# Optimization experiments

Hardware: AMD Instinct MI355X
Metric: run time of the kernel (lower is better)

Reference implementation:

```python
import jax, jax.numpy as jnp
import numpy as np

L_SEG, M_CHEB, MODES1, MODES2 = 4, 8, 16, 16


def _cft(signals, t_coords, f_points, L, M):
    # signals: [N, C, n] real; returns (real, imag) each [N, C, F]
    n = signals.shape[-1]
    seg_len = 1.0 / L
    starts = jnp.linspace(0.0, 1.0, L + 1)[:-1]                      # [L]
    k = jnp.arange(M, dtype=jnp.float32)
    nodes = -jnp.cos((2.0 * k + 1.0) * jnp.pi / (2.0 * M))           # [M]
    T = jnp.cos(k[:, None] * jnp.arccos(nodes)[None, :])             # [M(k), M(m)]
    w_prime = f_points * (2.0 * jnp.pi * (seg_len / 2.0))            # [F]
    angle = nodes[:, None] * w_prime[None, :]                        # [M, F]
    # quad weights (index k is reused as node index m downstream, as in original)
    Wr = (T @ jnp.cos(angle)) * (seg_len / 2.0)                      # [M, F]
    Wi = (T @ (-jnp.sin(angle))) * (seg_len / 2.0)                   # [M, F] (sign = -1, forward)
    # chebyshev sample points for all segments at once
    t_seg = starts[:, None] + (seg_len / 2.0) * (nodes[None, :] + 1.0)   # [L, M]
    right = jnp.clip(jnp.searchsorted(t_coords, t_seg), 0, n - 1)
    left = jnp.clip(right - 1, 0, n - 1)
    tl, tr = t_coords[left], t_coords[right]
    denom = jnp.where(tr - tl < 1e-8, 1.0, tr - tl)
    wr = (t_seg - tl) / denom
    wl = 1.0 - wr
    seg_sig = wl * signals[..., left] + wr * signals[..., right]     # [N, C, L, M]
    Sr = jnp.einsum('nclm,mf->nclf', seg_sig, Wr)
    Si = jnp.einsum('nclm,mf->nclf', seg_sig, Wi)
    phase = -2.0 * jnp.pi * starts[:, None] * f_points[None, :]      # [L, F]
    cr, ci = jnp.cos(phase), jnp.sin(phase)
    real = jnp.sum(Sr * cr - Si * ci, axis=2)
    imag = jnp.sum(Sr * ci + Si * cr, axis=2)
    return real, imag


def _cft2d(x, m1, m2, L, M):
    B, C, H, W = x.shape
    tw = jnp.linspace(0.0, 1.0, W)
    fw = jnp.fft.rfftfreq(W, d=1.0 / W)[:m2].astype(jnp.float32)
    xr = x.transpose(0, 2, 1, 3).reshape(B * H, C, W)
    r, i = _cft(xr, tw, fw, L, M)                                    # [B*H, C, m2]
    r = r.reshape(B, H, C, m2).transpose(0, 2, 1, 3)                 # [B, C, H, m2]
    i = i.reshape(B, H, C, m2).transpose(0, 2, 1, 3)
    th = jnp.linspace(0.0, 1.0, H)
    fh = jnp.fft.fftfreq(H, d=1.0 / H).astype(jnp.float32)
    hidx = np.concatenate([np.arange(0, m1 // 2), np.arange(H - (m1 - m1 // 2), H)])
    fsel = fh[hidx]
    rh = r.transpose(0, 3, 1, 2).reshape(B * m2, C, H)
    ih = i.transpose(0, 3, 1, 2).reshape(B * m2, C, H)
    rr, ri = _cft(rh, th, fsel, L, M)
    ir, ii = _cft(ih, th, fsel, L, M)
    real = (rr - ii).reshape(B, m2, C, m1).transpose(0, 2, 3, 1)     # [B, C, m1, m2]
    imag = (ri + ir).reshape(B, m2, C, m1).transpose(0, 2, 3, 1)
    return real, imag


def setup_inputs() -> dict:
    key = jax.random.key(0)
    ks = jax.random.split(key, 6)
    B, C, O, H, W = 32, 64, 64, 128, 128
    m1, m2 = MODES1, MODES2
    scale = 1.0 / (C * O)
    x = jax.random.normal(ks[0], (B, C, H, W), jnp.float32)
    w1 = scale * jax.random.uniform(ks[1], (C, O, m1, m2, 2), jnp.float32)
    w2 = scale * jax.random.uniform(ks[2], (C, O, m1, m2, 2), jnp.float32)
    d_in = C * (m1 // 4) * (m2 // 4) * 2
    hid = (C + O) * 2
    lin1_w = jax.random.normal(ks[3], (d_in, hid), jnp.float32) * 0.02
    lin1_b = jnp.zeros((hid,), jnp.float32)
    lin2_w = jax.random.normal(ks[4], (hid, O), jnp.float32) * 0.02
    lin2_b = jnp.zeros((O,), jnp.float32)
    return dict(x=x, w1=w1, w2=w2, lin1_w=lin1_w, lin1_b=lin1_b, lin2_w=lin2_w, lin2_b=lin2_b)


def reference(x, w1, w2, lin1_w, lin1_b, lin2_w, lin2_b):
    m1, m2 = MODES1, MODES2
    B, C, H, W = x.shape
    O = w1.shape[1]
    # FNO spectral conv
    xf = jnp.fft.rfft2(x)                                            # [B, C, H, W//2+1]
    w1c = w1[..., 0] + 1j * w1[..., 1]
    w2c = w2[..., 0] + 1j * w2[..., 1]
    out_ft = jnp.zeros((B, O, H, W // 2 + 1), jnp.complex64)
    out_ft = out_ft.at[:, :, :m1, :m2].set(
        jnp.einsum('bixy,ioxy->boxy', xf[:, :, :m1, :m2], w1c))
    out_ft = out_ft.at[:, :, H - m1:, :m2].set(
        jnp.einsum('bixy,ioxy->boxy', xf[:, :, H - m1:, :m2], w2c))
    x_fno = jnp.fft.irfft2(out_ft, s=(H, W))
    # Chebyshev-quadrature CFT correction path
    cr, ci = _cft2d(x, m1 // 4, m2 // 4, L_SEG, M_CHEB)              # [B, C, m1//4, m2//4]
    flat = jnp.stack([cr, ci], axis=-1).reshape(B, -1)               # view_as_real + flatten(1)
    h = jax.nn.gelu(flat @ lin1_w + lin1_b, approximate=False)
    corr = h @ lin2_w + lin2_b                                       # [B, O]
    return x_fno + corr[:, :, None, None]
```

## Files before the change

kernel.cpp:

```cpp
#include <hip/hip_runtime.h>
#include <math.h>

#define PI_F 3.14159265358979323846f
#define TWO_PI_F 6.28318530717958647692f

constexpr int Bn = 32, Cn = 64, On = 64, Hn = 128, Wn = 128;

constexpr size_t WSO_FLAT  = 0;
constexpr size_t WSO_CORR  = 65536;
constexpr size_t WSO_HS    = 67584;
constexpr size_t WSO_BIG   = 81920;
constexpr size_t SZ_QTR    = (size_t)2097152;
constexpr size_t WSO_XF    = WSO_BIG + SZ_QTR;
constexpr size_t WSO_OUTFT = WSO_BIG + 4 * SZ_QTR;

struct Tabs {
  float ktw[128][40];
  float cfth[128][8];
};

constexpr double D_PI = 3.14159265358979323846;

constexpr double d_red(double x) {
  while (x >  D_PI) x -= 2.0 * D_PI;
  while (x < -D_PI) x += 2.0 * D_PI;
  return x;
}
constexpr double d_sin(double x) {
  x = d_red(x);
  double x2 = x * x, t = x, s = x;
  for (int n = 1; n <= 10; n++) { t *= -x2 / (double)((2 * n) * (2 * n + 1)); s += t; }
  return s;
}
constexpr double d_cos(double x) {
  x = d_red(x);
  double x2 = x * x, t = 1.0, s = 1.0;
  for (int n = 1; n <= 10; n++) { t *= -x2 / (double)((2 * n - 1) * (2 * n)); s += t; }
  return s;
}

constexpr Tabs make_tabs() {
  Tabs T{};
  double twc[128] = {}, tws[128] = {};
  for (int r = 0; r < 128; r++) {
    double a = 2.0 * D_PI * (double)r / 128.0;
    twc[r] = d_cos(a); tws[r] = d_sin(a);
  }
  for (int kx = 0; kx < 16; kx++)
    for (int w = 0; w < 128; w++) {
      int r = (kx * w) & 127;
      T.ktw[w][2 * kx]     = (float)twc[r];
      T.ktw[w][2 * kx + 1] = (float)(-tws[r]);
    }
  double node[8] = {}, theta[8] = {};
  for (int m = 0; m < 8; m++) { theta[m] = (2.0 * m + 1.0) * D_PI / 16.0; node[m] = -d_cos(theta[m]); }
  double Tch[8][8] = {};
  for (int k = 0; k < 8; k++)
    for (int m = 0; m < 8; m++) Tch[k][m] = d_cos((double)k * (D_PI - theta[m]));
  int LE[4][8] = {}, RI[4][8] = {};
  float WL[4][8] = {}, WR[4][8] = {};
  for (int l = 0; l < 4; l++)
    for (int m = 0; m < 8; m++) {
      float tseg = (float)(0.25 * (double)l + 0.125 * (node[m] + 1.0));
      int ri = (int)(tseg * 127.0f) - 2; if (ri < 0) ri = 0;
      while (ri < 127 && ((float)ri * (1.0f / 127.0f)) < tseg) ri++;
      int le = ri - 1; if (le < 0) le = 0;
      float tl = (float)le * (1.0f / 127.0f), tr = (float)ri * (1.0f / 127.0f);
      float den = (tr - tl < 1e-8f) ? 1.0f : (tr - tl);
      float wr = (tseg - tl) / den;
      LE[l][m] = le; RI[l][m] = ri; WR[l][m] = wr; WL[l][m] = 1.0f - wr;
    }
  for (int p = 0; p < 2; p++)
    for (int f = 0; f < 4; f++) {
      double fval = (p == 0) ? (double)f
                             : ((f == 0) ? 0.0 : (f == 1) ? 1.0 : (f == 2) ? -2.0 : -1.0);
      double wp = fval * (2.0 * D_PI * 0.125);
      double Wr[8] = {}, Wi[8] = {};
      for (int k = 0; k < 8; k++) {
        double sr = 0.0, si = 0.0;
        for (int m = 0; m < 8; m++) {
          sr += Tch[k][m] * d_cos(node[m] * wp);
          si += Tch[k][m] * (-d_sin(node[m] * wp));
        }
        Wr[k] = sr * 0.125; Wi[k] = si * 0.125;
      }
      for (int l = 0; l < 4; l++) {
        double ph = -2.0 * D_PI * (0.25 * (double)l) * fval;
        double cr = d_cos(ph), ci = d_sin(ph);
        for (int m = 0; m < 8; m++) {
          double coefR = Wr[m] * cr - Wi[m] * ci;
          double coefI = Wr[m] * ci + Wi[m] * cr;
          int le = LE[l][m], ri = RI[l][m];
          if (p == 0) {
            T.ktw[le][32 + f] += (float)(WL[l][m] * coefR);
            T.ktw[le][36 + f] += (float)(WL[l][m] * coefI);
            T.ktw[ri][32 + f] += (float)(WR[l][m] * coefR);
            T.ktw[ri][36 + f] += (float)(WR[l][m] * coefI);
          } else {
            T.cfth[le][f]     += (float)(WL[l][m] * coefR);
            T.cfth[le][4 + f] += (float)(WL[l][m] * coefI);
            T.cfth[ri][f]     += (float)(WR[l][m] * coefR);
            T.cfth[ri][4 + f] += (float)(WR[l][m] * coefI);
          }
        }
      }
    }
  return T;
}

constexpr unsigned short cf2bf(float f) {
  unsigned u = __builtin_bit_cast(unsigned, f);
  u += 0x7FFFu + ((u >> 16) & 1u);
  return (unsigned short)(u >> 16);
}
constexpr float cbf2f(unsigned short h) {
  return __builtin_bit_cast(float, (unsigned)h << 16);
}

struct CfthT { float v[128][8]; };
constexpr CfthT make_cfth() {
  CfthT C{};
  Tabs T = make_tabs();
  for (int h = 0; h < 128; h++)
    for (int q = 0; q < 8; q++) C.v[h][q] = T.cfth[h][q];
  return C;
}
__constant__ CfthT g_cfth = make_cfth();

struct alignas(16) BTab {
  unsigned short v[4][2][3][64][8];
};
constexpr BTab make_btab() {
  BTab B{};
  Tabs T = make_tabs();
  for (int ks = 0; ks < 4; ks++)
    for (int jt = 0; jt < 3; jt++)
      for (int lane = 0; lane < 64; lane++)
        for (int j = 0; j < 8; j++) {
          int col = jt * 16 + (lane & 15);
          int k = ks * 32 + (lane >> 4) * 8 + j;
          float val = (col < 40) ? T.ktw[k][col] : 0.0f;
          unsigned short h = cf2bf(val);
          B.v[ks][0][jt][lane][j] = h;
          B.v[ks][1][jt][lane][j] = cf2bf(val - cbf2f(h));
        }
  return B;
}
__constant__ BTab g_btab = make_btab();

struct alignas(16) TBTab {
  unsigned short v[4][8][2][64][8];
};
constexpr TBTab make_tbtab() {
  TBTab T{};
  double twc[128] = {}, tws[128] = {};
  for (int r = 0; r < 128; r++) {
    double a = 2.0 * D_PI * (double)r / 128.0;
    twc[r] = d_cos(a); tws[r] = d_sin(a);
  }
  for (int mt = 0; mt < 4; mt++)
    for (int ks = 0; ks < 8; ks++)
      for (int lane = 0; lane < 64; lane++)
        for (int js = 0; js < 8; js++) {
          int m = mt * 16 + (lane & 15);
          int j = m & 31, ri = m >> 5;
          int k = ks * 32 + (lane >> 4) * 8 + js;
          int h = k >> 1, u = k & 1;
          int ky = (j < 16) ? j : j + 96;
          int idx = (ky * h) & 127;
          double c = twc[idx], s = tws[idx];
          double val = (ri == 0) ? ((u == 0) ? c : s)
                                 : ((u == 0) ? -s : c);
          float f = (float)val;
          unsigned short hi = cf2bf(f);
          T.v[mt][ks][0][lane][js] = hi;
          T.v[mt][ks][1][lane][js] = cf2bf(f - cbf2f(hi));
        }
  return T;
}
__constant__ TBTab g_tbtab = make_tbtab();

struct alignas(16) W1Tab {
  unsigned short v[16][2][2][64][8];
};
constexpr W1Tab make_w1tab() {
  W1Tab T{};
  double twc[128] = {}, tws[128] = {};
  for (int r = 0; r < 128; r++) {
    double a = 2.0 * D_PI * (double)r / 128.0;
    twc[r] = d_cos(a); tws[r] = d_sin(a);
  }
  for (int mt = 0; mt < 16; mt++)
    for (int ks = 0; ks < 2; ks++)
      for (int lane = 0; lane < 64; lane++)
        for (int j = 0; j < 8; j++) {
          int r = mt * 16 + (lane & 15);
          int k = ks * 32 + (lane >> 4) * 8 + j;
          int jj = k >> 1, u = k & 1;
          int ky = (jj < 16) ? jj : jj + 96;
          int h = r & 127;
          int idx = (ky * h) & 127;
          double c = twc[idx], s = tws[idx];
          double val = (r < 128) ? ((u == 0) ? c : -s)
                                 : ((u == 0) ? s : c);
          float f = (float)(val * (1.0 / 128.0));
          unsigned short hi = cf2bf(f);
          T.v[mt][ks][0][lane][j] = hi;
          T.v[mt][ks][1][lane][j] = cf2bf(f - cbf2f(hi));
        }
  return T;
}
__constant__ W1Tab g_w1tab = make_w1tab();

struct alignas(16) W2Tab {
  unsigned short v[8][2][64][8];
};
constexpr W2Tab make_w2tab() {
  W2Tab T{};
  double twc[128] = {}, tws[128] = {};
  for (int r = 0; r < 128; r++) {
    double a = 2.0 * D_PI * (double)r / 128.0;
    twc[r] = d_cos(a); tws[r] = d_sin(a);
  }
  for (int nt = 0; nt < 8; nt++)
    for (int lane = 0; lane < 64; lane++)
      for (int j = 0; j < 8; j++) {
        int w = nt * 16 + (lane & 15);
        int k = (lane >> 4) * 8 + j;
        int kx = k >> 1, u = k & 1;
        double val;
        if (kx == 0) val = (u == 0) ? 1.0 : 0.0;
        else {
          int idx = (kx * w) & 127;
          val = (u == 0) ? 2.0 * twc[idx] : -2.0 * tws[idx];
        }
        float f = (float)(val * (1.0 / 128.0));
        unsigned short hi = cf2bf(f);
        T.v[nt][0][lane][j] = hi;
        T.v[nt][1][lane][j] = cf2bf(f - cbf2f(hi));
      }
  return T;
}
__constant__ W2Tab g_w2tab = make_w2tab();

typedef __attribute__((ext_vector_type(8))) __bf16 bf16x8;
typedef __attribute__((ext_vector_type(8))) unsigned short ushort8;
typedef __attribute__((ext_vector_type(4))) float f32x4;

__device__ __forceinline__ unsigned short f2bf(float f) {
  unsigned u = __builtin_bit_cast(unsigned, f);
  u += 0x7FFFu + ((u >> 16) & 1u);
  return (unsigned short)(u >> 16);
}
__device__ __forceinline__ float bf2f(unsigned short h) {
  return __builtin_bit_cast(float, (unsigned)h << 16);
}

__global__ __launch_bounds__(256) void k_fwd(const float* __restrict__ x,
                                             float* __restrict__ xf,
                                             float* __restrict__ flat) {
  __shared__ float xs[64][132];
  __shared__ float xwl[128][34];
  __shared__ float cftl[128][9];
  __shared__ float cpart[8][33];
  int t = threadIdx.x;
  int lane = t & 63, wid = t >> 6;
  int bc = blockIdx.x;
  const float* xb = x + (size_t)bc * 16384;
  int r = lane & 15, kg = lane >> 4;

  #pragma unroll
  for (int ch = 0; ch < 2; ch++) {
    const float4* s4 = reinterpret_cast<const float4*>(xb + ch * 8192);
    float4 st[8];
    #pragma unroll
    for (int i = 0; i < 8; i++) st[i] = s4[t + i * 256];
    #pragma unroll
    for (int i = 0; i < 8; i++) {
      int idx = t + i * 256, row = idx >> 5, c4 = idx & 31;
      *reinterpret_cast<float4*>(&xs[row][c4 * 4]) = st[i];
    }
    __syncthreads();

    bf16x8 ahi[4], alo[4];
    #pragma unroll
    for (int ks = 0; ks < 4; ks++) {
      const float* p = &xs[wid * 16 + r][kg * 8 + ks * 32];
      float4 v0 = *reinterpret_cast<const float4*>(p);
      float4 v1 = *reinterpret_cast<const float4*>(p + 4);
      float xv[8] = {v0.x, v0.y, v0.z, v0.w, v1.x, v1.y, v1.z, v1.w};
      ushort8 hu, lu;
      #pragma unroll
      for (int j = 0; j < 8; j++) {
        unsigned short h = f2bf(xv[j]);
        hu[j] = h;
        lu[j] = f2bf(xv[j] - bf2f(h));
      }
      ahi[ks] = __builtin_bit_cast(bf16x8, hu);
      alo[ks] = __builtin_bit_cast(bf16x8, lu);
    }
    #pragma unroll
    for (int jt = 0; jt < 3; jt++) {
      f32x4 acc = {0.f, 0.f, 0.f, 0.f};
      #pragma unroll
      for (int ks = 0; ks < 4; ks++) {
        bf16x8 bhi = __builtin_bit_cast(bf16x8,
            *reinterpret_cast<const ushort8*>(&g_btab.v[ks][0][jt][lane][0]));
        bf16x8 blo = __builtin_bit_cast(bf16x8,
            *reinterpret_cast<const ushort8*>(&g_btab.v[ks][1][jt][lane][0]));
        acc = __builtin_amdgcn_mfma_f32_16x16x32_bf16(ahi[ks], bhi, acc, 0, 0, 0);
        acc = __builtin_amdgcn_mfma_f32_16x16x32_bf16(alo[ks], bhi, acc, 0, 0, 0);
        acc = __builtin_amdgcn_mfma_f32_16x16x32_bf16(ahi[ks], blo, acc, 0, 0, 0);
      }
      int col = lane & 15, rq = lane >> 4;
      #pragma unroll
      for (int i = 0; i < 4; i++) {
        int rl = ch * 64 + wid * 16 + rq * 4 + i;
        if (jt < 2) xwl[rl][jt * 16 + col] = acc[i];
        else if (col < 8) cftl[rl][col] = acc[i];
      }
    }
    __syncthreads();
  }

  {
    int o = t & 31, seg = t >> 5;
    int f1 = o >> 3, f2 = (o >> 1) & 3, ri = o & 1;
    float acc2 = 0.f;
    #pragma unroll
    for (int hh = 0; hh < 16; hh++) {
      int h = seg * 16 + hh;
      float rr = cftl[h][f2], im = cftl[h][4 + f2];
      float kr = g_cfth.v[h][f1], ki = g_cfth.v[h][4 + f1];
      float e0 = ri ? ki : kr;
      float e1 = ri ? kr : -ki;
      acc2 = fmaf(rr, e0, fmaf(im, e1, acc2));
    }
    cpart[seg][o] = acc2;
  }

  {
    int kx = lane & 15, g = lane >> 4;
    f32x4 accA = {0.f, 0.f, 0.f, 0.f};
    f32x4 accB = {0.f, 0.f, 0.f, 0.f};
    #pragma unroll
    for (int ks2 = 0; ks2 < 4; ks2++) {
      #pragma unroll
      for (int half = 0; half < 2; half++) {
        int ks = half * 4 + ks2;
        int h0 = ks * 16 + g * 4;
        ushort8 bhU, blU;
        #pragma unroll
        for (int rr = 0; rr < 4; rr++) {
          float2 p = *reinterpret_cast<const float2*>(&xwl[h0 + rr][2 * kx]);
          unsigned short hx = f2bf(p.x);
          bhU[2 * rr] = hx; blU[2 * rr] = f2bf(p.x - bf2f(hx));
          unsigned short hy = f2bf(p.y);
          bhU[2 * rr + 1] = hy; blU[2 * rr + 1] = f2bf(p.y - bf2f(hy));
        }
        bf16x8 bhi = __builtin_bit_cast(bf16x8, bhU);
        bf16x8 blo = __builtin_bit_cast(bf16x8, blU);
        bf16x8 thi = __builtin_bit_cast(bf16x8,
            *reinterpret_cast<const ushort8*>(&g_tbtab.v[wid][ks][0][lane][0]));
        bf16x8 tlo = __builtin_bit_cast(bf16x8,
            *reinterpret_cast<const ushort8*>(&g_tbtab.v[wid][ks][1][lane][0]));
        f32x4& acc3 = half ? accB : accA;
        acc3 = __builtin_amdgcn_mfma_f32_16x16x32_bf16(thi, bhi, acc3, 0, 0, 0);
        acc3 = __builtin_amdgcn_mfma_f32_16x16x32_bf16(tlo, bhi, acc3, 0, 0, 0);
        acc3 = __builtin_amdgcn_mfma_f32_16x16x32_bf16(thi, blo, acc3, 0, 0, 0);
      }
    }
    f32x4 accS = accA + accB;
    #pragma unroll
    for (int i = 0; i < 4; i++) {
      int m = wid * 16 + (lane >> 4) * 4 + i;
      int j = m & 31, ri = m >> 5;
      xf[((size_t)bc * 32 + j) * 32 + kx * 2 + ri] = accS[i];
    }
  }
  __syncthreads();

  if (t < 32) {
    float s = 0.f;
    #pragma unroll
    for (int seg = 0; seg < 8; seg++) s += cpart[seg][t];
    int b = bc >> 6, c = bc & 63;
    int f1 = t >> 3, f2 = (t >> 1) & 3, ri = t & 1;
    flat[(size_t)b * 2048 + ((c * 4 + f1) * 4 + f2) * 2 + ri] = s;
  }
}

__global__ __launch_bounds__(256) void k_mlp1(const float* __restrict__ flat,
                                              const float* __restrict__ w1,
                                              const float* __restrict__ b1,
                                              float* __restrict__ hs) {
  __shared__ float part[4][64];
  int bid = blockIdx.x;
  int b = bid >> 2, oc = bid & 3;
  int t = threadIdx.x;
  int ol = t & 63, kc = t >> 6;
  int o = oc * 64 + ol;
  const float* fb = flat + (size_t)b * 2048 + kc * 512;
  const float* wb = w1 + (size_t)(kc * 512) * 256 + o;
  float acc = 0.f;
  for (int k = 0; k < 512; k++) acc = fmaf(fb[k], wb[(size_t)k * 256], acc);
  part[kc][ol] = acc;
  __syncthreads();
  if (t < 64) {
    float a = part[0][t] + part[1][t] + part[2][t] + part[3][t] + b1[oc * 64 + t];
    hs[(size_t)b * 256 + oc * 64 + t] = 0.5f * a * (1.0f + erff(a * 0.70710678118654752f));
  }
}

__global__ void k_mlp2(const float* __restrict__ hs,
                       const float* __restrict__ w2,
                       const float* __restrict__ b2,
                       float* __restrict__ corr) {
  int b = blockIdx.x, t = threadIdx.x;
  const float* hb = hs + (size_t)b * 256;
  float acc = b2[t];
  for (int k = 0; k < 256; k++) acc = fmaf(hb[k], w2[(size_t)k * 64 + t], acc);
  corr[(size_t)b * 64 + t] = acc;
}

__global__ __launch_bounds__(256) void k_stageC(const float* __restrict__ xf,
                                                const float* __restrict__ w1,
                                                const float* __restrict__ w2,
                                                float* __restrict__ outft) {
  __shared__ float xfs[64 * 32];
  int bid = blockIdx.x;
  int sw = (bid & 7) * 128 + (bid >> 3);
  int j = sw >> 5, b = sw & 31;
  int t = threadIdx.x;
  #pragma unroll
  for (int k2 = 0; k2 < 4; k2++) {
    int id = t + k2 * 256;
    int c = id >> 4, kxi = id & 15;
    const float2 v = *reinterpret_cast<const float2*>(
        xf + (((size_t)b * 64 + c) * 32 + j) * 32 + kxi * 2);
    reinterpret_cast<float2*>(xfs)[id] = v;
  }
  __syncthreads();
  int kx = t & 15, og = t >> 4;
  const float* wsel = (j < 16) ? w1 : w2;
  int jr = (j < 16) ? j : j - 16;
  float aR[4], aI[4];
  #pragma unroll
  for (int i = 0; i < 4; i++) { aR[i] = 0.f; aI[i] = 0.f; }
  for (int c = 0; c < 64; c++) {
    float xr = xfs[c * 32 + kx * 2], xi = xfs[c * 32 + kx * 2 + 1];
    #pragma unroll
    for (int i = 0; i < 4; i++) {
      int o = og * 4 + i;
      const float2 wv = *reinterpret_cast<const float2*>(
          wsel + ((((size_t)c * 64 + o) * 16 + jr) * 16 + kx) * 2);
      aR[i] = fmaf(xr, wv.x, fmaf(-xi, wv.y, aR[i]));
      aI[i] = fmaf(xr, wv.y, fmaf(xi, wv.x, aI[i]));
    }
  }
  int boff = (j >> 4) * 512 + ((((j >> 2) & 3) << 4) | kx) * 8 + (j & 3) * 2;
  #pragma unroll
  for (int i = 0; i < 4; i++) {
    int o = og * 4 + i;
    float2* dst = reinterpret_cast<float2*>(outft + (size_t)(b * 64 + o) * 1024 + boff);
    *dst = make_float2(aR[i], aI[i]);
  }
}

__global__ __launch_bounds__(256) void k_stageDE(const float* __restrict__ outft,
                                                 const float* __restrict__ corr,
                                                 float* __restrict__ out) {
  __shared__ float Yl[256 * 17];
  int t = threadIdx.x;
  int lane = t & 63, wid = t >> 6;
  int bo = blockIdx.x;
  const float* src = outft + (size_t)bo * 1024;

  bf16x8 shi[2], slo[2];
  #pragma unroll
  for (int ks = 0; ks < 2; ks++) {
    float4 v0 = *reinterpret_cast<const float4*>(src + ks * 512 + lane * 8);
    float4 v1 = *reinterpret_cast<const float4*>(src + ks * 512 + lane * 8 + 4);
    float xv[8] = {v0.x, v0.y, v0.z, v0.w, v1.x, v1.y, v1.z, v1.w};
    ushort8 hu, lu;
    #pragma unroll
    for (int j = 0; j < 8; j++) {
      unsigned short h = f2bf(xv[j]);
      hu[j] = h;
      lu[j] = f2bf(xv[j] - bf2f(h));
    }
    shi[ks] = __builtin_bit_cast(bf16x8, hu);
    slo[ks] = __builtin_bit_cast(bf16x8, lu);
  }

  #pragma unroll
  for (int mtl = 0; mtl < 4; mtl++) {
    int mt = wid * 4 + mtl;
    f32x4 acc = {0.f, 0.f, 0.f, 0.f};
    #pragma unroll
    for (int ks = 0; ks < 2; ks++) {
      bf16x8 whi = __builtin_bit_cast(bf16x8,
          *reinterpret_cast<const ushort8*>(&g_w1tab.v[mt][ks][0][lane][0]));
      bf16x8 wlo = __builtin_bit_cast(bf16x8,
          *reinterpret_cast<const ushort8*>(&g_w1tab.v[mt][ks][1][lane][0]));
      acc = __builtin_amdgcn_mfma_f32_16x16x32_bf16(whi, shi[ks], acc, 0, 0, 0);
      acc = __builtin_amdgcn_mfma_f32_16x16x32_bf16(wlo, shi[ks], acc, 0, 0, 0);
      acc = __builtin_amdgcn_mfma_f32_16x16x32_bf16(whi, slo[ks], acc, 0, 0, 0);
    }
    #pragma unroll
    for (int i = 0; i < 4; i++)
      Yl[(mt * 16 + (lane >> 4) * 4 + i) * 17 + (lane & 15)] = acc[i];
  }
  __syncthreads();

  float corrv = corr[bo];
  float* obase = out + (size_t)bo * 16384;

  #pragma unroll
  for (int mtl = 0; mtl < 2; mtl++) {
    int mt2 = wid * 2 + mtl;
    int h = mt2 * 16 + (lane & 15);
    ushort8 ahiU, aloU;
    #pragma unroll
    for (int j = 0; j < 8; j++) {
      int k = (lane >> 4) * 8 + j;
      float v = Yl[((k & 1) * 128 + h) * 17 + (k >> 1)];
      unsigned short hi = f2bf(v);
      ahiU[j] = hi;
      aloU[j] = f2bf(v - bf2f(hi));
    }
    bf16x8 ahi = __builtin_bit_cast(bf16x8, ahiU);
    bf16x8 alo = __builtin_bit_cast(bf16x8, aloU);
    #pragma unroll
    for (int nt = 0; nt < 8; nt++) {
      bf16x8 bhi = __builtin_bit_cast(bf16x8,
          *reinterpret_cast<const ushort8*>(&g_w2tab.v[nt][0][lane][0]));
      bf16x8 blo = __builtin_bit_cast(bf16x8,
          *reinterpret_cast<const ushort8*>(&g_w2tab.v[nt][1][lane][0]));
      f32x4 acc = {corrv, corrv, corrv, corrv};
      acc = __builtin_amdgcn_mfma_f32_16x16x32_bf16(ahi, bhi, acc, 0, 0, 0);
      acc = __builtin_amdgcn_mfma_f32_16x16x32_bf16(alo, bhi, acc, 0, 0, 0);
      acc = __builtin_amdgcn_mfma_f32_16x16x32_bf16(ahi, blo, acc, 0, 0, 0);
      #pragma unroll
      for (int i = 0; i < 4; i++)
        obase[(mt2 * 16 + (lane >> 4) * 4 + i) * 128 + nt * 16 + (lane & 15)] = acc[i];
    }
  }
}

extern "C" void kernel_launch(void* const* d_in, const int* in_sizes, int n_in,
                              void* d_out, int out_size, void* d_ws, size_t ws_size,
                              hipStream_t stream) {
  const float* x   = (const float*)d_in[0];
  const float* w1  = (const float*)d_in[1];
  const float* w2  = (const float*)d_in[2];
  const float* l1w = (const float*)d_in[3];
  const float* l1b = (const float*)d_in[4];
  const float* l2w = (const float*)d_in[5];
  const float* l2b = (const float*)d_in[6];
  float* out = (float*)d_out;
  float* ws  = (float*)d_ws;

  float* flat  = ws + WSO_FLAT;
  float* corr  = ws + WSO_CORR;
  float* hs    = ws + WSO_HS;
  float* xf    = ws + WSO_XF;
  float* outft = ws + WSO_OUTFT;

  k_fwd<<<dim3(2048), dim3(256), 0, stream>>>(x, xf, flat);
  k_mlp1<<<dim3(128), dim3(256), 0, stream>>>(flat, l1w, l1b, hs);
  k_mlp2<<<dim3(32), dim3(64), 0, stream>>>(hs, l2w, l2b, corr);
  k_stageC<<<dim3(1024), dim3(256), 0, stream>>>(xf, w1, w2, outft);
  k_stageDE<<<dim3(2048), dim3(256), 0, stream>>>(outft, corr, out);
}
```

Baseline: 148.5 us.

## Restructure forward kernel with direct global-to-LDS loads, 512 threads, pre-split bf16

The forward kernel now loads the whole 128x128 tile in one pass with global_load_lds into a swizzled LDS buffer and runs 512 threads (8 waves) instead of looping over two 64-row halves with register staging. The hi/lo bf16 split of the intermediate W-transform is done once at write time and stored packed, so the H-stage MFMA loop only unpacks it. The CFT reduction now runs on the upper 256 threads while the lower 256 run the H-stage MFMAs. This removes a sync round and redundant conversions, but LDS use rises to about 64KB+ per block, which may cut occupancy.

```diff
diff --git a/kernel.cpp b/kernel.cpp
--- a/kernel.cpp
+++ b/kernel.cpp
@@ -248,46 +248,49 @@
 typedef __attribute__((ext_vector_type(4))) float f32x4;
 
 __device__ __forceinline__ unsigned short f2bf(float f) {
-  unsigned u = __builtin_bit_cast(unsigned, f);
-  u += 0x7FFFu + ((u >> 16) & 1u);
-  return (unsigned short)(u >> 16);
+  return __builtin_bit_cast(unsigned short, (__bf16)f);
 }
 __device__ __forceinline__ float bf2f(unsigned short h) {
-  return __builtin_bit_cast(float, (unsigned)h << 16);
-}
-
-__global__ __launch_bounds__(256) void k_fwd(const float* __restrict__ x,
+  return (float)__builtin_bit_cast(__bf16, h);
+}
+
+__device__ __forceinline__ void gload16(const float* g, float* l) {
+  __builtin_amdgcn_global_load_lds(
+      (const __attribute__((address_space(1))) unsigned*)g,
+      (__attribute__((address_space(3))) unsigned*)l, 16, 0, 0);
+}
+
+__global__ __launch_bounds__(512) void k_fwd(const float* __restrict__ x,
                                              float* __restrict__ xf,
                                              float* __restrict__ flat) {
-  __shared__ float xs[64][132];
-  __shared__ float xwl[128][34];
+  __shared__ float xs[16384];
+  __shared__ unsigned xwlp[128][34];
   __shared__ float cftl[128][9];
   __shared__ float cpart[8][33];
   int t = threadIdx.x;
   int lane = t & 63, wid = t >> 6;
   int bc = blockIdx.x;
   const float* xb = x + (size_t)bc * 16384;
-  int r = lane & 15, kg = lane >> 4;
-
-  #pragma unroll
-  for (int ch = 0; ch < 2; ch++) {
-    const float4* s4 = reinterpret_cast<const float4*>(xb + ch * 8192);
-    float4 st[8];
-    #pragma unroll
-    for (int i = 0; i < 8; i++) st[i] = s4[t + i * 256];
-    #pragma unroll
-    for (int i = 0; i < 8; i++) {
-      int idx = t + i * 256, row = idx >> 5, c4 = idx & 31;
-      *reinterpret_cast<float4*>(&xs[row][c4 * 4]) = st[i];
-    }
-    __syncthreads();
-
+
+  #pragma unroll
+  for (int i = 0; i < 8; i++) {
+    int s = (wid * 8 + i) * 64 + lane;
+    int R = s >> 5, p = s & 31;
+    const float* g = xb + R * 128 + ((p ^ (R & 31)) << 2);
+    gload16(g, &xs[(wid * 8 + i) * 256]);
+  }
+  asm volatile("s_waitcnt vmcnt(0)" ::: "memory");
+  __builtin_amdgcn_sched_barrier(0);
+
+  {
+    int r = lane & 15, kg = lane >> 4;
+    int R = wid * 16 + r, key = R & 31;
+    const float* rowb = xs + R * 128;
     bf16x8 ahi[4], alo[4];
     #pragma unroll
     for (int ks = 0; ks < 4; ks++) {
-      const float* p = &xs[wid * 16 + r][kg * 8 + ks * 32];
-      float4 v0 = *reinterpret_cast<const float4*>(p);
-      float4 v1 = *reinterpret_cast<const float4*>(p + 4);
+      float4 v0 = *reinterpret_cast<const float4*>(rowb + (((kg * 2 + ks * 8)     ^ key) << 2));
+      float4 v1 = *reinterpret_cast<const float4*>(rowb + (((kg * 2 + ks * 8 + 1) ^ key) << 2));
       float xv[8] = {v0.x, v0.y, v0.z, v0.w, v1.x, v1.y, v1.z, v1.w};
       ushort8 hu, lu;
       #pragma unroll
@@ -315,31 +318,22 @@
       int col = lane & 15, rq = lane >> 4;
       #pragma unroll
       for (int i = 0; i < 4; i++) {
-        int rl = ch * 64 + wid * 16 + rq * 4 + i;
-        if (jt < 2) xwl[rl][jt * 16 + col] = acc[i];
-        else if (col < 8) cftl[rl][col] = acc[i];
-      }
-    }
-    __syncthreads();
-  }
-
-  {
-    int o = t & 31, seg = t >> 5;
-    int f1 = o >> 3, f2 = (o >> 1) & 3, ri = o & 1;
-    float acc2 = 0.f;
-    #pragma unroll
-    for (int hh = 0; hh < 16; hh++) {
-      int h = seg * 16 + hh;
-      float rr = cftl[h][f2], im = cftl[h][4 + f2];
-      float kr = g_cfth.v[h][f1], ki = g_cfth.v[h][4 + f1];
-      float e0 = ri ? ki : kr;
-      float e1 = ri ? kr : -ki;
-      acc2 = fmaf(rr, e0, fmaf(im, e1, acc2));
-    }
-    cpart[seg][o] = acc2;
-  }
-
-  {
+        int rl = wid * 16 + rq * 4 + i;
+        float v = acc[i];
+        if (jt < 2) {
+          unsigned short hi = f2bf(v);
+          unsigned short lo = f2bf(v - bf2f(hi));
+          xwlp[rl][jt * 16 + col] = ((unsigned)lo << 16) | (unsigned)hi;
+        } else if (col < 8) {
+          cftl[rl][col] = v;
+        }
+      }
+    }
+  }
+  __syncthreads();
+
+  if (t < 256) {
+    int w4 = t >> 6;
     int kx = lane & 15, g = lane >> 4;
     f32x4 accA = {0.f, 0.f, 0.f, 0.f};
     f32x4 accB = {0.f, 0.f, 0.f, 0.f};
@@ -352,18 +346,18 @@
         ushort8 bhU, blU;
         #pragma unroll
         for (int rr = 0; rr < 4; rr++) {
-          float2 p = *reinterpret_cast<const float2*>(&xwl[h0 + rr][2 * kx]);
-          unsigned short hx = f2bf(p.x);
-          bhU[2 * rr] = hx; blU[2 * rr] = f2bf(p.x - bf2f(hx));
-          unsigned short hy = f2bf(p.y);
-          bhU[2 * rr + 1] = hy; blU[2 * rr + 1] = f2bf(p.y - bf2f(hy));
+          uint2 p = *reinterpret_cast<const uint2*>(&xwlp[h0 + rr][2 * kx]);
+          bhU[2 * rr]     = (unsigned short)(p.x & 0xFFFFu);
+          blU[2 * rr]     = (unsigned short)(p.x >> 16);
+          bhU[2 * rr + 1] = (unsigned short)(p.y & 0xFFFFu);
+          blU[2 * rr + 1] = (unsigned short)(p.y >> 16);
         }
         bf16x8 bhi = __builtin_bit_cast(bf16x8, bhU);
         bf16x8 blo = __builtin_bit_cast(bf16x8, blU);
         bf16x8 thi = __builtin_bit_cast(bf16x8,
-            *reinterpret_cast<const ushort8*>(&g_tbtab.v[wid][ks][0][lane][0]));
+            *reinterpret_cast<const ushort8*>(&g_tbtab.v[w4][ks][0][lane][0]));
         bf16x8 tlo = __builtin_bit_cast(bf16x8,
-            *reinterpret_cast<const ushort8*>(&g_tbtab.v[wid][ks][1][lane][0]));
+            *reinterpret_cast<const ushort8*>(&g_tbtab.v[w4][ks][1][lane][0]));
         f32x4& acc3 = half ? accB : accA;
         acc3 = __builtin_amdgcn_mfma_f32_16x16x32_bf16(thi, bhi, acc3, 0, 0, 0);
         acc3 = __builtin_amdgcn_mfma_f32_16x16x32_bf16(tlo, bhi, acc3, 0, 0, 0);
@@ -373,20 +367,34 @@
     f32x4 accS = accA + accB;
     #pragma unroll
     for (int i = 0; i < 4; i++) {
-      int m = wid * 16 + (lane >> 4) * 4 + i;
+      int m = w4 * 16 + (lane >> 4) * 4 + i;
       int j = m & 31, ri = m >> 5;
       xf[((size_t)bc * 32 + j) * 32 + kx * 2 + ri] = accS[i];
     }
+  } else {
+    int o = t & 31, seg = (t >> 5) - 8;
+    int f1 = o >> 3, f2 = (o >> 1) & 3, ri = o & 1;
+    float acc2 = 0.f;
+    #pragma unroll
+    for (int hh = 0; hh < 16; hh++) {
+      int h = seg * 16 + hh;
+      float rr = cftl[h][f2], im = cftl[h][4 + f2];
+      float kr = g_cfth.v[h][f1], ki = g_cfth.v[h][4 + f1];
+      float e0 = ri ? ki : kr;
+      float e1 = ri ? kr : -ki;
+      acc2 = fmaf(rr, e0, fmaf(im, e1, acc2));
+    }
+    cpart[seg][o] = acc2;
   }
   __syncthreads();
 
   if (t < 32) {
-    float s = 0.f;
-    #pragma unroll
-    for (int seg = 0; seg < 8; seg++) s += cpart[seg][t];
+    float sum = 0.f;
+    #pragma unroll
+    for (int seg = 0; seg < 8; seg++) sum += cpart[seg][t];
     int b = bc >> 6, c = bc & 63;
     int f1 = t >> 3, f2 = (t >> 1) & 3, ri = t & 1;
-    flat[(size_t)b * 2048 + ((c * 4 + f1) * 4 + f2) * 2 + ri] = s;
+    flat[(size_t)b * 2048 + ((c * 4 + f1) * 4 + f2) * 2 + ri] = sum;
   }
 }
 
@@ -567,7 +575,7 @@
   float* xf    = ws + WSO_XF;
   float* outft = ws + WSO_OUTFT;
 
-  k_fwd<<<dim3(2048), dim3(256), 0, stream>>>(x, xf, flat);
+  k_fwd<<<dim3(2048), dim3(512), 0, stream>>>(x, xf, flat);
   k_mlp1<<<dim3(128), dim3(256), 0, stream>>>(flat, l1w, l1b, hs);
   k_mlp2<<<dim3(32), dim3(64), 0, stream>>>(hs, l2w, l2b, corr);
   k_stageC<<<dim3(1024), dim3(256), 0, stream>>>(xf, w1, w2, outft);
```

Measured after the change: 150.9 us. No clear change (+1.7%).
